# Kernel optimization log

Measured on AMD Instinct MI355X. Metric: run time of the kernel, lower is better.

Reference implementation:

```python
import jax, jax.numpy as jnp
import numpy as np

N = 100000   # nodes
E = 1600000  # edges (avg degree 16)
D = 128      # input feature dim
H = 64       # hidden dim (hard-coded in Sage.__init__)
C = 40       # output classes


def setup_inputs() -> dict:
    key = jax.random.key(0)
    ks = jax.random.split(key, 9)
    s_in = 1.0 / np.sqrt(D)
    s_h = 1.0 / np.sqrt(H)
    return {
        "x": jax.random.normal(ks[0], (N, D), jnp.float32),
        "edge_index": jax.random.randint(ks[1], (2, E), 0, N, dtype=jnp.int64),
        # SAGEConv params: lin_l acts on aggregated neighbors (carries bias),
        # lin_r acts on the root/self features (no bias), per PyG defaults.
        "W1_l": jax.random.uniform(ks[2], (D, H), jnp.float32, -s_in, s_in),
        "W1_r": jax.random.uniform(ks[3], (D, H), jnp.float32, -s_in, s_in),
        "b1": jax.random.uniform(ks[4], (H,), jnp.float32, -s_in, s_in),
        "W2_l": jax.random.uniform(ks[5], (H, C), jnp.float32, -s_h, s_h),
        "W2_r": jax.random.uniform(ks[6], (H, C), jnp.float32, -s_h, s_h),
        "b2": jax.random.uniform(ks[7], (C,), jnp.float32, -s_h, s_h),
    }


def _sage_conv(x, src, dst, W_l, W_r, b):
    # mean-aggregate neighbor features at destination nodes
    msg = x[src]                                             # [E, F] gather
    summed = jax.ops.segment_sum(msg, dst, num_segments=N)   # [N, F]
    deg = jax.ops.segment_sum(jnp.ones((src.shape[0],), x.dtype), dst,
                              num_segments=N)                # [N]
    agg = summed / jnp.maximum(deg, 1.0)[:, None]
    return agg @ W_l + x @ W_r + b


def reference(x, edge_index, W1_l, W1_r, b1, W2_l, W2_r, b2):
    src, dst = edge_index[0], edge_index[1]
    h = _sage_conv(x, src, dst, W1_l, W1_r, b1)
    h = jax.nn.relu(h)
    # F.dropout(training=False) in eval mode -> identity
    out = _sage_conv(h, src, dst, W2_l, W2_r, b2)
    return jax.nn.log_softmax(out, axis=1)
```

## Files before the change

### kernel.cpp

```cpp
#include <hip/hip_runtime.h>

__device__ __forceinline__ float bf2f(unsigned short u) {
  union { unsigned int i; float f; } c; c.i = ((unsigned int)u) << 16; return c.f;
}
__device__ __forceinline__ unsigned short f2bf(float f) {
  union { float f; unsigned int i; } c; c.f = f;
  unsigned int x = c.i;
  return (unsigned short)((x + 0x7fffu + ((x >> 16) & 1u)) >> 16);
}
__device__ __forceinline__ float lo16(unsigned int w) { return bf2f((unsigned short)(w & 0xffffu)); }
__device__ __forceinline__ float hi16(unsigned int w) { return bf2f((unsigned short)(w >> 16)); }

#define DD 128
#define HH 64
#define CC 40
#define NBUCK 512
#define NCHUNK 256
#define NSCAT 128
#define MAXNPB 256
#define NR 4
#define ECAP 6144

using bf16x8 = __attribute__((ext_vector_type(8))) short;
using f32x4  = __attribute__((ext_vector_type(4))) float;

__global__ __launch_bounds__(256) void detect_prepw_hist(
    const unsigned int* e32u, const unsigned int* x32, int* flags,
    const void* W1l, const void* W1r, const void* b1,
    const void* W2l, const void* W2r, const void* b2,
    unsigned short* Wb1, unsigned short* Wb2, float* b1f, float* b2f,
    const int* e32, int E, int N, unsigned mulM, int* histG) {
  __shared__ int cnt[NBUCK * NR];
  int tid = threadIdx.x;
  int b = blockIdx.x;

  if (b == 0) {
    unsigned int v = 0;
    for (int i = tid; i < 4096; i += 256) v |= e32u[2 * i + 1];
    int c2 = 0;
    for (int i = tid; i < 4096; i += 256) {
      unsigned int w = x32[i];
      unsigned int expo = (w >> 7) & 0xffu;
      unsigned short lo = (unsigned short)(w & 0xffffu);
      if (lo == 0 || (expo >= 100u && expo <= 133u)) c2++;
    }
    cnt[tid] = (int)v; cnt[256 + tid] = c2; __syncthreads();
    for (int s = 128; s > 0; s >>= 1) {
      if (tid < s) { cnt[tid] |= cnt[tid + s]; cnt[256 + tid] += cnt[256 + tid + s]; }
      __syncthreads();
    }
    if (tid == 0) {
      flags[0] = (cnt[0] == 0) ? 1 : 0;
      flags[1] = (cnt[256] < 2048) ? 1 : 0;
    }
    return;
  }

  if (b <= 2) {
    const unsigned int* w32 = (const unsigned int*)W1l;
    int c2 = 0;
    for (int i = tid; i < 4096; i += 256) {
      unsigned int w = w32[i];
      unsigned int expo = (w >> 7) & 0xffu;
      unsigned short lo = (unsigned short)(w & 0xffffu);
      if (lo == 0 || (expo >= 100u && expo <= 133u)) c2++;
    }
    cnt[tid] = c2; __syncthreads();
    for (int s = 128; s > 0; s >>= 1) {
      if (tid < s) cnt[tid] += cnt[tid + s];
      __syncthreads();
    }
    int isf = (cnt[0] < 2048) ? 1 : 0;
    auto rd = [&](const void* p, int i) -> float {
      return isf ? ((const float*)p)[i] : bf2f(((const unsigned short*)p)[i]);
    };
    if (b == 1) {
      for (int idx = tid; idx < 128 * 128; idx += 256) {
        int n = idx >> 7, k = idx & 127;
        float v = (n < HH) ? rd(W1l, k * HH + n) : rd(W1r, k * HH + (n - HH));
        Wb1[idx] = f2bf(v);
      }
    } else {
      for (int idx = tid; idx < 48 * 128; idx += 256) {
        int n = idx >> 7, k = idx & 127;
        float v = 0.f;
        if (n < CC) v = (k < HH) ? rd(W2l, k * CC + n) : rd(W2r, (k - HH) * CC + n);
        Wb2[idx] = f2bf(v);
      }
      if (tid < HH) b1f[tid] = rd(b1, tid);
      if (tid < CC) b2f[tid] = rd(b2, tid);
    }
    return;
  }

  int hb = b - 3;
  unsigned int v = 0;
  for (int i = tid; i < 4096; i += 256) v |= e32u[2 * i + 1];
  cnt[tid] = (int)v; __syncthreads();
  for (int s = 128; s > 0; s >>= 1) {
    if (tid < s) cnt[tid] |= cnt[tid + s];
    __syncthreads();
  }
  int isI64 = (cnt[0] == 0) ? 1 : 0;
  __syncthreads();
  for (int i = tid; i < NBUCK * NR; i += 256) cnt[i] = 0;
  __syncthreads();
  int rep = tid & (NR - 1);
  int chunk = (E + NCHUNK - 1) / NCHUNK;
  int e0 = hb * chunk, e1 = min(e0 + chunk, E);
  for (int i = e0 + tid; i < e1; i += 256) {
    int d = isI64 ? e32[2 * (E + i)] : e32[E + i];
    d = min(max(d, 0), N - 1);
    int bk = (int)__umulhi((unsigned)d, mulM);
    atomicAdd(&cnt[bk * NR + rep], 1);
  }
  __syncthreads();
  for (int i = tid; i < NBUCK; i += 256)
    histG[i * NCHUNK + hb] =
        cnt[i * NR] + cnt[i * NR + 1] + cnt[i * NR + 2] + cnt[i * NR + 3];
}

__global__ __launch_bounds__(256) void scanA(const int* histG, int* ohist, int* bsum) {
  __shared__ int t[NCHUNK];
  int b = blockIdx.x, tid = threadIdx.x;
  int v = histG[b * NCHUNK + tid];
  t[tid] = v; __syncthreads();
  for (int st = 1; st < NCHUNK; st <<= 1) {
    int u = (tid >= st) ? t[tid - st] : 0;
    __syncthreads();
    t[tid] += u;
    __syncthreads();
  }
  ohist[b * NCHUNK + tid] = t[tid] - v;
  if (tid == NCHUNK - 1) bsum[b] = t[tid];
}

__global__ __launch_bounds__(512) void scanB(const int* bsum, int* bbase,
                                             int* row_ptr, int N, int E) {
  __shared__ int t[NBUCK];
  int tid = threadIdx.x;
  int v = bsum[tid];
  t[tid] = v; __syncthreads();
  for (int st = 1; st < NBUCK; st <<= 1) {
    int u = (tid >= st) ? t[tid - st] : 0;
    __syncthreads();
    t[tid] += u;
    __syncthreads();
  }
  bbase[tid] = t[tid] - v;
  if (tid == 0) { bbase[NBUCK] = E; row_ptr[N] = E; }
}

__global__ __launch_bounds__(256) void scat_or_t1(
    const int* e32, int E, int N, const int* flags, int nodesPerB,
    unsigned mulM, const int* ohist, const int* bbase, unsigned* ebuf,
    const void* xraw, const unsigned short* Wb1, const float* b1f,
    unsigned short* t1, unsigned short* s1, int T1B) {
  __shared__ int cur[NBUCK];
  int b = blockIdx.x;
  int tid = threadIdx.x;

  if (b < NSCAT) {
    for (int i = tid; i < NBUCK; i += 256)
      cur[i] = ohist[i * NCHUNK + 2 * b] + bbase[i];
    __syncthreads();
    int isI64 = flags[0];
    int chunk = (E + NCHUNK - 1) / NCHUNK;
    int e0 = 2 * b * chunk, e1 = min(e0 + 2 * chunk, E);
    for (int i = e0 + tid; i < e1; i += 256) {
      int s, d;
      if (isI64) { s = e32[2 * i]; d = e32[2 * (E + i)]; }
      else       { s = e32[i];     d = e32[E + i]; }
      s = min(max(s, 0), N - 1);
      d = min(max(d, 0), N - 1);
      int bk = (int)__umulhi((unsigned)d, mulM);
      int ld = d - bk * nodesPerB;
      int p = atomicAdd(&cur[bk], 1);
      ebuf[p] = ((unsigned)ld << 17) | (unsigned)s;
    }
    return;
  }

  int t = b - NSCAT;
  if (t >= T1B) return;
  int lane = tid & 63, wv = tid >> 6;
  int nb = t * 64 + wv * 16;
  int oc = lane & 15, kgrp = lane >> 4;
  int node = min(nb + oc, N - 1);
  f32x4 acc[8];
#pragma unroll
  for (int i = 0; i < 8; i++) acc[i] = (f32x4){0.f, 0.f, 0.f, 0.f};

  if (flags[1]) {
    const float4* x4 = (const float4*)xraw;
#pragma unroll
    for (int kb = 0; kb < 4; kb++) {
      int k0 = kb * 32 + kgrp * 8;
      float4 a0 = x4[(size_t)node * 32 + (k0 >> 2)];
      float4 a1 = x4[(size_t)node * 32 + (k0 >> 2) + 1];
      bf16x8 af;
      af[0] = (short)f2bf(a0.x); af[1] = (short)f2bf(a0.y);
      af[2] = (short)f2bf(a0.z); af[3] = (short)f2bf(a0.w);
      af[4] = (short)f2bf(a1.x); af[5] = (short)f2bf(a1.y);
      af[6] = (short)f2bf(a1.z); af[7] = (short)f2bf(a1.w);
#pragma unroll
      for (int nblk = 0; nblk < 8; nblk++) {
        bf16x8 bfr = *(const bf16x8*)&Wb1[(nblk * 16 + oc) * 128 + k0];
        acc[nblk] = __builtin_amdgcn_mfma_f32_16x16x32_bf16(af, bfr, acc[nblk], 0, 0, 0);
      }
    }
  } else {
    const unsigned short* x16 = (const unsigned short*)xraw;
#pragma unroll
    for (int kb = 0; kb < 4; kb++) {
      int k0 = kb * 32 + kgrp * 8;
      bf16x8 af = *(const bf16x8*)&x16[(size_t)node * 128 + k0];
#pragma unroll
      for (int nblk = 0; nblk < 8; nblk++) {
        bf16x8 bfr = *(const bf16x8*)&Wb1[(nblk * 16 + oc) * 128 + k0];
        acc[nblk] = __builtin_amdgcn_mfma_f32_16x16x32_bf16(af, bfr, acc[nblk], 0, 0, 0);
      }
    }
  }

  int r0 = kgrp * 4;
#pragma unroll
  for (int nblk = 0; nblk < 8; nblk++) {
    float bias = (nblk >= 4) ? b1f[(nblk - 4) * 16 + oc] : 0.f;
#pragma unroll
    for (int r = 0; r < 4; r++) {
      int nn = nb + r0 + r;
      if (nn < N) {
        if (nblk < 4)
          t1[(size_t)nn * HH + nblk * 16 + oc] = f2bf(acc[nblk][r]);
        else
          s1[(size_t)nn * HH + (nblk - 4) * 16 + oc] = f2bf(acc[nblk][r] + bias);
      }
    }
  }
}

__global__ __launch_bounds__(256) void bktB(
    const unsigned* ebuf, const int* bbase,
    int nodesPerB, int* row_ptr, float* invd, int* col, int N) {
  __shared__ unsigned ecache[ECAP];
  __shared__ int cnt[MAXNPB];
  __shared__ int sA[256];
  int b = blockIdx.x;
  int tid = threadIdx.x;
  int base_node = b * nodesPerB;
  int nn = min(nodesPerB, N - base_node);
  if (nn <= 0) return;
  int eb0 = bbase[b], eb1 = bbase[b + 1];
  int nE = eb1 - eb0;
  const unsigned* ee = ebuf + eb0;
  bool useL = (nE <= ECAP);
  for (int i = tid; i < nn; i += 256) cnt[i] = 0;
  __syncthreads();
  if (useL) {
    for (int i = tid; i < nE; i += 256) {
      unsigned v = ee[i];
      ecache[i] = v;
      atomicAdd(&cnt[v >> 17], 1);
    }
  } else {
    for (int i = tid; i < nE; i += 256) atomicAdd(&cnt[ee[i] >> 17], 1);
  }
  __syncthreads();
  int deg = (tid < nn) ? cnt[tid] : 0;
  if (tid < nn) invd[base_node + tid] = 1.0f / (float)max(deg, 1);
  sA[tid] = deg;
  __syncthreads();
  for (int st = 1; st < 256; st <<= 1) {
    int t = (tid >= st) ? sA[tid - st] : 0;
    __syncthreads();
    sA[tid] += t;
    __syncthreads();
  }
  int run = eb0 + sA[tid] - deg;
  __syncthreads();
  if (tid < nn) {
    row_ptr[base_node + tid] = run;
    cnt[tid] = run;
  }
  __syncthreads();
  if (useL) {
    for (int i = tid; i < nE; i += 256) {
      unsigned v = ecache[i];
      int p = atomicAdd(&cnt[v >> 17], 1);
      col[p] = (int)(v & 0x1FFFFu);
    }
  } else {
    for (int i = tid; i < nE; i += 256) {
      unsigned v = ee[i];
      int p = atomicAdd(&cnt[v >> 17], 1);
      col[p] = (int)(v & 0x1FFFFu);
    }
  }
}

__device__ __forceinline__ void gather_seg(const uint4* t8, const int* col,
                                           int s0, int s1, int r, int c,
                                           float acc[8]) {
  for (int base = s0; base < s1; base += 4) {
    int i = base + r;
    bool g = (i < s1);
    int nb = g ? col[i] : 0;
    uint4 v = make_uint4(0, 0, 0, 0);
    if (g) v = t8[(size_t)nb * 8 + c];
    acc[0] += lo16(v.x); acc[1] += hi16(v.x);
    acc[2] += lo16(v.y); acc[3] += hi16(v.y);
    acc[4] += lo16(v.z); acc[5] += hi16(v.z);
    acc[6] += lo16(v.w); acc[7] += hi16(v.w);
  }
}

__global__ __launch_bounds__(256) void aggregate1(const unsigned short* t1,
                                                  const unsigned short* s1,
                                                  const int* row_ptr, const float* invd,
                                                  const int* col, unsigned short* h, int N) {
  int wave = threadIdx.x >> 6, lane = threadIdx.x & 63;
  int ns = lane >> 5, r = (lane >> 3) & 3, c = lane & 7;
  int n = blockIdx.x * 8 + wave * 2 + ns;
  if (n >= N) return;
  int s0 = row_ptr[n], s1e = row_ptr[n + 1];
  float acc[8] = {0, 0, 0, 0, 0, 0, 0, 0};
  gather_seg((const uint4*)t1, col, s0, s1e, r, c, acc);
#pragma unroll
  for (int m = 8; m <= 16; m <<= 1)
#pragma unroll
    for (int i = 0; i < 8; i++) acc[i] += __shfl_xor(acc[i], m, 64);

  if (r == 0) {
    float id = invd[n];
    uint4 sv = ((const uint4*)s1)[(size_t)n * 8 + c];
    float s[8] = {lo16(sv.x), hi16(sv.x), lo16(sv.y), hi16(sv.y),
                  lo16(sv.z), hi16(sv.z), lo16(sv.w), hi16(sv.w)};
    unsigned int o[4];
#pragma unroll
    for (int i = 0; i < 4; i++) {
      float a0 = fmaxf(acc[2 * i] * id + s[2 * i], 0.f);
      float a1 = fmaxf(acc[2 * i + 1] * id + s[2 * i + 1], 0.f);
      o[i] = (unsigned int)f2bf(a0) | ((unsigned int)f2bf(a1) << 16);
    }
    ((uint4*)h)[(size_t)n * 8 + c] = make_uint4(o[0], o[1], o[2], o[3]);
  }
}

__global__ __launch_bounds__(256) void agg2f(const unsigned short* h,
                                             const int* row_ptr, const float* invd,
                                             const int* col,
                                             const unsigned short* Wb2,
                                             const float* b2f,
                                             float* out, int N) {
  __shared__ unsigned lds[64 * 33];
  int tid = threadIdx.x, wv = tid >> 6, lane = tid & 63;
  int ns = lane >> 5, r = (lane >> 3) & 3, c = lane & 7;
  int nb = blockIdx.x * 64;
  const uint4* h8 = (const uint4*)h;

  for (int rr = 0; rr < 8; rr++) {
    int ln = wv * 16 + rr * 2 + ns;
    int n = nb + ln;
    float acc[8] = {0, 0, 0, 0, 0, 0, 0, 0};
    int s0 = 0, s1e = 0;
    if (n < N) { s0 = row_ptr[n]; s1e = row_ptr[n + 1]; }
    gather_seg(h8, col, s0, s1e, r, c, acc);
#pragma unroll
    for (int m = 8; m <= 16; m <<= 1)
#pragma unroll
      for (int i = 0; i < 8; i++) acc[i] += __shfl_xor(acc[i], m, 64);
    if (r == 0) {
      float id = (n < N) ? invd[n] : 0.f;
#pragma unroll
      for (int q = 0; q < 4; q++) {
        unsigned u = (unsigned)f2bf(acc[2 * q] * id) |
                     ((unsigned)f2bf(acc[2 * q + 1] * id) << 16);
        lds[ln * 33 + c * 4 + q] = u;
      }
    }
  }
  __syncthreads();

  int oc = lane & 15, kgrp = lane >> 4;
  int noderow = wv * 16 + oc;
  int node = min(nb + noderow, N - 1);
  f32x4 acc3[3];
#pragma unroll
  for (int i = 0; i < 3; i++) acc3[i] = (f32x4){0.f, 0.f, 0.f, 0.f};

#pragma unroll
  for (int kb = 0; kb < 4; kb++) {
    int k0 = kb * 32 + kgrp * 8;
    bf16x8 af;
    if (kb < 2) {
      union { unsigned u[4]; bf16x8 v; } cv;
      int base = noderow * 33 + (k0 >> 1);
      cv.u[0] = lds[base]; cv.u[1] = lds[base + 1];
      cv.u[2] = lds[base + 2]; cv.u[3] = lds[base + 3];
      af = cv.v;
    } else {
      af = *(const bf16x8*)&h[(size_t)node * HH + (k0 - 64)];
    }
#pragma unroll
    for (int nblk = 0; nblk < 3; nblk++) {
      bf16x8 bfr = *(const bf16x8*)&Wb2[(nblk * 16 + oc) * 128 + k0];
      acc3[nblk] = __builtin_amdgcn_mfma_f32_16x16x32_bf16(af, bfr, acc3[nblk], 0, 0, 0);
    }
  }

#pragma unroll
  for (int nblk = 0; nblk < 3; nblk++) {
    int cc = nblk * 16 + oc;
    float bias = (cc < CC) ? b2f[cc] : 0.f;
#pragma unroll
    for (int rg = 0; rg < 4; rg++) acc3[nblk][rg] += bias;
  }

#pragma unroll
  for (int rg = 0; rg < 4; rg++) {
    int nn = nb + wv * 16 + kgrp * 4 + rg;
    float m = -INFINITY;
#pragma unroll
    for (int nblk = 0; nblk < 3; nblk++)
      if (nblk * 16 + oc < CC) m = fmaxf(m, acc3[nblk][rg]);
    for (int off = 1; off <= 8; off <<= 1) m = fmaxf(m, __shfl_xor(m, off, 64));
    float s = 0.f;
#pragma unroll
    for (int nblk = 0; nblk < 3; nblk++)
      if (nblk * 16 + oc < CC) s += __expf(acc3[nblk][rg] - m);
    for (int off = 1; off <= 8; off <<= 1) s += __shfl_xor(s, off, 64);
    float lse = m + __logf(s);
    if (nn < N) {
#pragma unroll
      for (int nblk = 0; nblk < 3; nblk++) {
        int cc = nblk * 16 + oc;
        if (cc < CC) out[(size_t)nn * CC + cc] = acc3[nblk][rg] - lse;
      }
    }
  }
}

extern "C" void kernel_launch(void* const* d_in, const int* in_sizes, int n_in,
                              void* d_out, int out_size, void* d_ws, size_t ws_size,
                              hipStream_t stream) {
  const void* x   = d_in[0];
  const int*  e   = (const int*)d_in[1];
  const void* W1l = d_in[2];
  const void* W1r = d_in[3];
  const void* b1  = d_in[4];
  const void* W2l = d_in[5];
  const void* W2r = d_in[6];
  const void* b2  = d_in[7];
  float* out = (float*)d_out;

  const int N = in_sizes[0] / DD;
  const int E = in_sizes[1] / 2;
  const int nodesPerB = (N + NBUCK - 1) / NBUCK;
  const int nbuck = (N + nodesPerB - 1) / nodesPerB;
  const unsigned mulM =
      (unsigned)(((1ULL << 32) + (unsigned)nodesPerB - 1) / (unsigned)nodesPerB);
  const int T1B = (N + 63) / 64;

  char* w = (char*)d_ws;
  size_t off = 0;
  auto carve = [&](size_t bytes) -> void* {
    void* p = (void*)(w + off);
    off += (bytes + 255) & ~(size_t)255;
    return p;
  };
  int* col      = (int*)carve((size_t)E * 4);
  int* row_ptr  = (int*)carve(((size_t)N + 1) * 4);
  float* invd   = (float*)carve((size_t)N * 4);
  int* histG    = (int*)carve((size_t)NBUCK * NCHUNK * 4);
  int* ohist    = (int*)carve((size_t)NBUCK * NCHUNK * 4);
  int* bsum     = (int*)carve(NBUCK * 4);
  int* bbase    = (int*)carve((NBUCK + 1) * 4);
  int* flags    = (int*)carve(8);
  unsigned short* t1   = (unsigned short*)carve((size_t)N * HH * 2);
  unsigned short* s1   = (unsigned short*)carve((size_t)N * HH * 2);
  unsigned short* h    = (unsigned short*)carve((size_t)N * HH * 2);
  unsigned short* Wb1  = (unsigned short*)carve(128 * 128 * 2);
  unsigned short* Wb2  = (unsigned short*)carve(48 * 128 * 2);
  float* b1f   = (float*)carve(HH * sizeof(float));
  float* b2f   = (float*)carve(CC * sizeof(float));
  unsigned* ebuf = (unsigned*)carve((size_t)E * 4);
  (void)ws_size; (void)n_in; (void)out_size;

  detect_prepw_hist<<<3 + NCHUNK, 256, 0, stream>>>(
      (const unsigned int*)e, (const unsigned int*)x, flags,
      W1l, W1r, b1, W2l, W2r, b2, Wb1, Wb2, b1f, b2f,
      e, E, N, mulM, histG);
  scanA<<<NBUCK, NCHUNK, 0, stream>>>(histG, ohist, bsum);
  scanB<<<1, 512, 0, stream>>>(bsum, bbase, row_ptr, N, E);
  scat_or_t1<<<NSCAT + T1B, 256, 0, stream>>>(e, E, N, flags, nodesPerB,
                                              mulM, ohist, bbase, ebuf,
                                              x, Wb1, b1f, t1, s1, T1B);
  bktB<<<nbuck, 256, 0, stream>>>(ebuf, bbase, nodesPerB, row_ptr, invd, col, N);
  aggregate1<<<(N + 7) / 8, 256, 0, stream>>>(t1, s1, row_ptr, invd, col, h, N);
  agg2f<<<(N + 63) / 64, 256, 0, stream>>>(h, row_ptr, invd, col, Wb2, b2f, out, N);
}
```

Baseline: 279.5 us.

## Fuse CSR bucket build with layer-1 aggregation and stage x tile in LDS

Merges the per-bucket CSR construction kernel with the first-layer mean aggregation, so each bucket block gathers its own nodes right after writing col, using the in-LDS degree and offsets instead of reloading row_ptr/invd. This removes one kernel launch and the re-reading of row pointers. The t1 transform now loads x rows cooperatively with coalesced accesses into shared memory before the MFMA loop. The cost is that aggregation parallelism drops to nbuck blocks (up to 512) with serial rounds per block, which may underuse the GPU compared with N/8 blocks.

```diff
diff --git a/kernel.cpp b/kernel.cpp
--- a/kernel.cpp
+++ b/kernel.cpp
@@ -156,11 +156,12 @@
     unsigned mulM, const int* ohist, const int* bbase, unsigned* ebuf,
     const void* xraw, const unsigned short* Wb1, const float* b1f,
     unsigned short* t1, unsigned short* s1, int T1B) {
-  __shared__ int cur[NBUCK];
+  __shared__ unsigned short shmem[8192];
   int b = blockIdx.x;
   int tid = threadIdx.x;
 
   if (b < NSCAT) {
+    int* cur = (int*)shmem;
     for (int i = tid; i < NBUCK; i += 256)
       cur[i] = ohist[i * NCHUNK + 2 * b] + bbase[i];
     __syncthreads();
@@ -186,40 +187,40 @@
   int lane = tid & 63, wv = tid >> 6;
   int nb = t * 64 + wv * 16;
   int oc = lane & 15, kgrp = lane >> 4;
-  int node = min(nb + oc, N - 1);
-  f32x4 acc[8];
-#pragma unroll
-  for (int i = 0; i < 8; i++) acc[i] = (f32x4){0.f, 0.f, 0.f, 0.f};
+  unsigned short* xs = shmem + wv * 2048;
 
   if (flags[1]) {
     const float4* x4 = (const float4*)xraw;
 #pragma unroll
-    for (int kb = 0; kb < 4; kb++) {
-      int k0 = kb * 32 + kgrp * 8;
-      float4 a0 = x4[(size_t)node * 32 + (k0 >> 2)];
-      float4 a1 = x4[(size_t)node * 32 + (k0 >> 2) + 1];
-      bf16x8 af;
-      af[0] = (short)f2bf(a0.x); af[1] = (short)f2bf(a0.y);
-      af[2] = (short)f2bf(a0.z); af[3] = (short)f2bf(a0.w);
-      af[4] = (short)f2bf(a1.x); af[5] = (short)f2bf(a1.y);
-      af[6] = (short)f2bf(a1.z); af[7] = (short)f2bf(a1.w);
-#pragma unroll
-      for (int nblk = 0; nblk < 8; nblk++) {
-        bf16x8 bfr = *(const bf16x8*)&Wb1[(nblk * 16 + oc) * 128 + k0];
-        acc[nblk] = __builtin_amdgcn_mfma_f32_16x16x32_bf16(af, bfr, acc[nblk], 0, 0, 0);
-      }
+    for (int j = 0; j < 8; j++) {
+      int c = j * 64 + lane;
+      int node2 = min(nb + (c >> 5), N - 1);
+      float4 v = x4[(size_t)node2 * 32 + (c & 31)];
+      unsigned short* dst = &xs[c * 4];
+      dst[0] = f2bf(v.x); dst[1] = f2bf(v.y);
+      dst[2] = f2bf(v.z); dst[3] = f2bf(v.w);
     }
   } else {
     const unsigned short* x16 = (const unsigned short*)xraw;
 #pragma unroll
-    for (int kb = 0; kb < 4; kb++) {
-      int k0 = kb * 32 + kgrp * 8;
-      bf16x8 af = *(const bf16x8*)&x16[(size_t)node * 128 + k0];
-#pragma unroll
-      for (int nblk = 0; nblk < 8; nblk++) {
-        bf16x8 bfr = *(const bf16x8*)&Wb1[(nblk * 16 + oc) * 128 + k0];
-        acc[nblk] = __builtin_amdgcn_mfma_f32_16x16x32_bf16(af, bfr, acc[nblk], 0, 0, 0);
-      }
+    for (int j = 0; j < 4; j++) {
+      int c = j * 64 + lane;
+      int node2 = min(nb + (c >> 4), N - 1);
+      *(bf16x8*)&xs[c * 8] = *(const bf16x8*)&x16[(size_t)node2 * 128 + (c & 15) * 8];
+    }
+  }
+
+  f32x4 acc[8];
+#pragma unroll
+  for (int i = 0; i < 8; i++) acc[i] = (f32x4){0.f, 0.f, 0.f, 0.f};
+#pragma unroll
+  for (int kb = 0; kb < 4; kb++) {
+    int k0 = kb * 32 + kgrp * 8;
+    bf16x8 af = *(const bf16x8*)&xs[oc * 128 + k0];
+#pragma unroll
+    for (int nblk = 0; nblk < 8; nblk++) {
+      bf16x8 bfr = *(const bf16x8*)&Wb1[(nblk * 16 + oc) * 128 + k0];
+      acc[nblk] = __builtin_amdgcn_mfma_f32_16x16x32_bf16(af, bfr, acc[nblk], 0, 0, 0);
     }
   }
 
@@ -236,65 +237,6 @@
         else
           s1[(size_t)nn * HH + (nblk - 4) * 16 + oc] = f2bf(acc[nblk][r] + bias);
       }
-    }
-  }
-}
-
-__global__ __launch_bounds__(256) void bktB(
-    const unsigned* ebuf, const int* bbase,
-    int nodesPerB, int* row_ptr, float* invd, int* col, int N) {
-  __shared__ unsigned ecache[ECAP];
-  __shared__ int cnt[MAXNPB];
-  __shared__ int sA[256];
-  int b = blockIdx.x;
-  int tid = threadIdx.x;
-  int base_node = b * nodesPerB;
-  int nn = min(nodesPerB, N - base_node);
-  if (nn <= 0) return;
-  int eb0 = bbase[b], eb1 = bbase[b + 1];
-  int nE = eb1 - eb0;
-  const unsigned* ee = ebuf + eb0;
-  bool useL = (nE <= ECAP);
-  for (int i = tid; i < nn; i += 256) cnt[i] = 0;
-  __syncthreads();
-  if (useL) {
-    for (int i = tid; i < nE; i += 256) {
-      unsigned v = ee[i];
-      ecache[i] = v;
-      atomicAdd(&cnt[v >> 17], 1);
-    }
-  } else {
-    for (int i = tid; i < nE; i += 256) atomicAdd(&cnt[ee[i] >> 17], 1);
-  }
-  __syncthreads();
-  int deg = (tid < nn) ? cnt[tid] : 0;
-  if (tid < nn) invd[base_node + tid] = 1.0f / (float)max(deg, 1);
-  sA[tid] = deg;
-  __syncthreads();
-  for (int st = 1; st < 256; st <<= 1) {
-    int t = (tid >= st) ? sA[tid - st] : 0;
-    __syncthreads();
-    sA[tid] += t;
-    __syncthreads();
-  }
-  int run = eb0 + sA[tid] - deg;
-  __syncthreads();
-  if (tid < nn) {
-    row_ptr[base_node + tid] = run;
-    cnt[tid] = run;
-  }
-  __syncthreads();
-  if (useL) {
-    for (int i = tid; i < nE; i += 256) {
-      unsigned v = ecache[i];
-      int p = atomicAdd(&cnt[v >> 17], 1);
-      col[p] = (int)(v & 0x1FFFFu);
-    }
-  } else {
-    for (int i = tid; i < nE; i += 256) {
-      unsigned v = ee[i];
-      int p = atomicAdd(&cnt[v >> 17], 1);
-      col[p] = (int)(v & 0x1FFFFu);
     }
   }
 }
@@ -315,35 +257,100 @@
   }
 }
 
-__global__ __launch_bounds__(256) void aggregate1(const unsigned short* t1,
-                                                  const unsigned short* s1,
-                                                  const int* row_ptr, const float* invd,
-                                                  const int* col, unsigned short* h, int N) {
-  int wave = threadIdx.x >> 6, lane = threadIdx.x & 63;
+__global__ __launch_bounds__(256) void bktB_agg1(
+    const unsigned* ebuf, const int* bbase,
+    int nodesPerB, int* row_ptr, float* invd, int* col, int N,
+    const unsigned short* t1, const unsigned short* s1v, unsigned short* h) {
+  __shared__ unsigned ecache[ECAP];
+  __shared__ int cnt[MAXNPB];
+  __shared__ int degL[MAXNPB];
+  __shared__ int sA[256];
+  int b = blockIdx.x;
+  int tid = threadIdx.x;
+  int base_node = b * nodesPerB;
+  int nn = min(nodesPerB, N - base_node);
+  if (nn <= 0) return;
+  int eb0 = bbase[b], eb1 = bbase[b + 1];
+  int nE = eb1 - eb0;
+  const unsigned* ee = ebuf + eb0;
+  bool useL = (nE <= ECAP);
+  for (int i = tid; i < nn; i += 256) cnt[i] = 0;
+  __syncthreads();
+  if (useL) {
+    for (int i = tid; i < nE; i += 256) {
+      unsigned v = ee[i];
+      ecache[i] = v;
+      atomicAdd(&cnt[v >> 17], 1);
+    }
+  } else {
+    for (int i = tid; i < nE; i += 256) atomicAdd(&cnt[ee[i] >> 17], 1);
+  }
+  __syncthreads();
+  int deg = (tid < nn) ? cnt[tid] : 0;
+  if (tid < nn) {
+    invd[base_node + tid] = 1.0f / (float)max(deg, 1);
+    degL[tid] = deg;
+  }
+  sA[tid] = deg;
+  __syncthreads();
+  for (int st = 1; st < 256; st <<= 1) {
+    int t = (tid >= st) ? sA[tid - st] : 0;
+    __syncthreads();
+    sA[tid] += t;
+    __syncthreads();
+  }
+  int run = eb0 + sA[tid] - deg;
+  __syncthreads();
+  if (tid < nn) {
+    row_ptr[base_node + tid] = run;
+    cnt[tid] = run;
+  }
+  __syncthreads();
+  if (useL) {
+    for (int i = tid; i < nE; i += 256) {
+      unsigned v = ecache[i];
+      int p = atomicAdd(&cnt[v >> 17], 1);
+      col[p] = (int)(v & 0x1FFFFu);
+    }
+  } else {
+    for (int i = tid; i < nE; i += 256) {
+      unsigned v = ee[i];
+      int p = atomicAdd(&cnt[v >> 17], 1);
+      col[p] = (int)(v & 0x1FFFFu);
+    }
+  }
+  __syncthreads();
+
+  int lane = tid & 63, wv = tid >> 6;
   int ns = lane >> 5, r = (lane >> 3) & 3, c = lane & 7;
-  int n = blockIdx.x * 8 + wave * 2 + ns;
-  if (n >= N) return;
-  int s0 = row_ptr[n], s1e = row_ptr[n + 1];
-  float acc[8] = {0, 0, 0, 0, 0, 0, 0, 0};
-  gather_seg((const uint4*)t1, col, s0, s1e, r, c, acc);
-#pragma unroll
-  for (int m = 8; m <= 16; m <<= 1)
-#pragma unroll
-    for (int i = 0; i < 8; i++) acc[i] += __shfl_xor(acc[i], m, 64);
-
-  if (r == 0) {
-    float id = invd[n];
-    uint4 sv = ((const uint4*)s1)[(size_t)n * 8 + c];
-    float s[8] = {lo16(sv.x), hi16(sv.x), lo16(sv.y), hi16(sv.y),
-                  lo16(sv.z), hi16(sv.z), lo16(sv.w), hi16(sv.w)};
-    unsigned int o[4];
-#pragma unroll
-    for (int i = 0; i < 4; i++) {
-      float a0 = fmaxf(acc[2 * i] * id + s[2 * i], 0.f);
-      float a1 = fmaxf(acc[2 * i + 1] * id + s[2 * i + 1], 0.f);
-      o[i] = (unsigned int)f2bf(a0) | ((unsigned int)f2bf(a1) << 16);
-    }
-    ((uint4*)h)[(size_t)n * 8 + c] = make_uint4(o[0], o[1], o[2], o[3]);
+  const uint4* t8 = (const uint4*)t1;
+  int rounds = (nn + 7) / 8;
+  for (int rr = 0; rr < rounds; rr++) {
+    int ln = rr * 8 + wv * 2 + ns;
+    bool ok = (ln < nn);
+    int s1e = ok ? cnt[ln] : 0;
+    int s0 = ok ? (s1e - degL[ln]) : 0;
+    float acc[8] = {0, 0, 0, 0, 0, 0, 0, 0};
+    gather_seg(t8, col, s0, s1e, r, c, acc);
+#pragma unroll
+    for (int m = 8; m <= 16; m <<= 1)
+#pragma unroll
+      for (int i = 0; i < 8; i++) acc[i] += __shfl_xor(acc[i], m, 64);
+    if (ok && r == 0) {
+      int n = base_node + ln;
+      float id = 1.0f / (float)max(degL[ln], 1);
+      uint4 sv = ((const uint4*)s1v)[(size_t)n * 8 + c];
+      float sb[8] = {lo16(sv.x), hi16(sv.x), lo16(sv.y), hi16(sv.y),
+                     lo16(sv.z), hi16(sv.z), lo16(sv.w), hi16(sv.w)};
+      unsigned int o[4];
+#pragma unroll
+      for (int i = 0; i < 4; i++) {
+        float a0 = fmaxf(acc[2 * i] * id + sb[2 * i], 0.f);
+        float a1 = fmaxf(acc[2 * i + 1] * id + sb[2 * i + 1], 0.f);
+        o[i] = (unsigned int)f2bf(a0) | ((unsigned int)f2bf(a1) << 16);
+      }
+      ((uint4*)h)[(size_t)n * 8 + c] = make_uint4(o[0], o[1], o[2], o[3]);
+    }
   }
 }
 
@@ -496,7 +503,7 @@
   scat_or_t1<<<NSCAT + T1B, 256, 0, stream>>>(e, E, N, flags, nodesPerB,
                                               mulM, ohist, bbase, ebuf,
                                               x, Wb1, b1f, t1, s1, T1B);
-  bktB<<<nbuck, 256, 0, stream>>>(ebuf, bbase, nodesPerB, row_ptr, invd, col, N);
-  aggregate1<<<(N + 7) / 8, 256, 0, stream>>>(t1, s1, row_ptr, invd, col, h, N);
+  bktB_agg1<<<nbuck, 256, 0, stream>>>(ebuf, bbase, nodesPerB, row_ptr, invd, col, N,
+                                       t1, s1, h);
   agg2f<<<(N + 63) / 64, 256, 0, stream>>>(h, row_ptr, invd, col, Wb2, b2f, out, N);
 }
```

Measured after the change: 336.4 us. +20.4%, slower.
